# Kernel optimization log

Measured on AMD Instinct MI355X. Metric: run time of the kernel, lower is better.

Reference implementation:

```python
import jax, jax.numpy as jnp
import numpy as np

NF = 64      # feature channels of h
K = 3        # dynamic filter spatial size (padding=1 in source implies k=3)
FACTOR = 4   # pixel-unshuffle factor


def shuffle_down(x, f):
    # torch pixel_unshuffle: (B,C,H*f,W*f) -> (B,C*f*f,H,W)
    B, C, H, W = x.shape
    x = x.reshape(B, C, H // f, f, W // f, f)
    x = x.transpose(0, 1, 3, 5, 2, 4)
    return x.reshape(B, C * f * f, H // f, W // f)


def _patches3x3(x):
    # x: (B,C,H,W) -> (B,C,9,H,W): zero-padded 3x3 neighborhoods, row-major taps,
    # identical to the identity-filter grouped conv (im2col) in the source.
    H, W = x.shape[-2], x.shape[-1]
    xp = jnp.pad(x, ((0, 0), (0, 0), (1, 1), (1, 1)))
    shifts = [xp[:, :, dy:dy + H, dx:dx + W] for dy in range(K) for dx in range(K)]
    return jnp.stack(shifts, axis=2)


def setup_inputs() -> dict:
    key = jax.random.key(0)
    k1, k2, k3, k4 = jax.random.split(key, 4)
    B, H, W = 2, 256, 256
    h = jax.random.normal(k1, (B, NF, H, W), dtype=jnp.float32)
    i_t = jax.random.normal(k2, (B, 3, H * FACTOR, W * FACTOR), dtype=jnp.float32)
    conv_w = jax.random.normal(k3, (K * K, 3 * FACTOR ** 2, K, K), dtype=jnp.float32) * 0.05
    conv_b = jax.random.normal(k4, (K * K,), dtype=jnp.float32) * 0.05
    return {"h": h, "i_t": i_t, "conv_w": conv_w, "conv_b": conv_b}


def reference(h, i_t, conv_w, conv_b):
    # predict per-pixel 3x3 filters from the shuffled-down guidance frame
    x = shuffle_down(i_t, FACTOR)  # (B, 48, H, W)
    f = jax.lax.conv_general_dilated(
        x, conv_w, window_strides=(1, 1), padding=((1, 1), (1, 1)),
        dimension_numbers=("NCHW", "OIHW", "NCHW"))
    filters = jax.nn.relu(f + conv_b[None, :, None, None])  # (B, 9, H, W)

    # dynamic per-pixel conv: same 3x3 filter applied to every channel of h
    patches = _patches3x3(h)  # (B, nf, 9, H, W)
    out = jnp.einsum("bcfhw,bfhw->bchw", patches, filters)  # (B, nf, H, W)
    return out
```

## Files before the change

### kernel.cpp

```cpp
#include <hip/hip_runtime.h>

#define HSZ 256
#define WSZ 256
#define NFC 64
#define PLANE (HSZ * WSZ)

typedef __attribute__((ext_vector_type(8))) short short8;
typedef __attribute__((ext_vector_type(4))) float f32x4;

__device__ inline unsigned short f2bf(float f) {
    unsigned u = __builtin_bit_cast(unsigned, f);
    return (unsigned short)((u + 0x7fffu + ((u >> 16) & 1u)) >> 16);
}

__global__ __launch_bounds__(256, 3) void fused_dynfilter_v2(
    const float* __restrict__ hbuf,
    const float* __restrict__ i_t,
    const float* __restrict__ wbuf,
    const float* __restrict__ bias,
    float* __restrict__ out)
{
    __shared__ __align__(16) unsigned char smem[45504];
    unsigned short* const xs = (unsigned short*)smem;
    unsigned short* const lw = (unsigned short*)(smem + 36288);
    float* const lf = (float*)(smem + 36288);
    float* const hs = (float*)smem;

    const int tid  = threadIdx.x;
    const int X0   = blockIdx.x * 16;
    const int Y0   = blockIdx.y * 16;
    const int b    = blockIdx.z;
    const int lane = tid & 63;
    const int l15  = lane & 15;
    const int kg   = lane >> 4;
    const int wv   = tid >> 6;

    const float bv = (l15 < 9) ? bias[l15] : 0.f;
    const float* itb = i_t + (size_t)b * 3 * (PLANE * 16);

    {
#pragma unroll
        for (int g = 0; g < 2; ++g) {
            float4 lreg[8]; int sdst[8];
#pragma unroll
            for (int k = 0; k < 8; ++k) {
                const int v = tid + 256 * (g * 8 + k);
                const int sp = v / 12, t = v - sp * 12;
                const int c3 = t >> 2, fy = t & 3;
                const int ly = sp / 18, lx = sp - ly * 18;
                const int Y = Y0 - 1 + ly, X = X0 - 1 + lx;
                float4 val = make_float4(0.f, 0.f, 0.f, 0.f);
                if (v < 3888 && (unsigned)Y < HSZ && (unsigned)X < WSZ)
                    val = *(const float4*)(itb + ((size_t)c3 * 1024 + (4 * Y + fy)) * 1024 + 4 * X);
                lreg[k] = val;
                sdst[k] = (v < 3888) ? (sp * 56 + t * 4) : -1;
            }
#pragma unroll
            for (int k = 0; k < 8; ++k)
                if (sdst[k] >= 0) {
                    ushort4 u{f2bf(lreg[k].x), f2bf(lreg[k].y), f2bf(lreg[k].z), f2bf(lreg[k].w)};
                    *(ushort4*)(xs + sdst[k]) = u;
                }
        }
    }

    {
        float wreg[16]; int wdst[16];
#pragma unroll
        for (int k = 0; k < 16; ++k) {
            const int v = tid + 256 * k;
            float w = 0.f; int d = -1;
            if (v < 3888) {
                const int oc = v / 432, kc = v - 432 * oc;
                const int kk = kc / 48, ic = kc - 48 * kk;
                w = wbuf[oc * 432 + ic * 9 + kk];
                d = kc * 9 + oc;
            }
            wreg[k] = w; wdst[k] = d;
        }
#pragma unroll
        for (int k = 0; k < 16; ++k)
            if (wdst[k] >= 0) lw[wdst[k]] = f2bf(wreg[k]);
    }

    __syncthreads();

    short8 wf[14];
    {
        const int base = kg * 72 + l15;
#pragma unroll
        for (int kb = 0; kb < 14; ++kb) {
            unsigned short v8[8];
#pragma unroll
            for (int j = 0; j < 8; ++j)
                v8[j] = lw[base + (kb * 32 + j) * 9];
            if (kb == 13 && kg >= 2) {
#pragma unroll
                for (int j = 0; j < 8; ++j) v8[j] = 0;
            }
            short8 w;
#pragma unroll
            for (int j = 0; j < 8; ++j) w[j] = (short)v8[j];
            wf[kb] = w;
        }
    }

    f32x4 acc[4];
#pragma unroll
    for (int t = 0; t < 4; ++t) acc[t] = (f32x4){0.f, 0.f, 0.f, 0.f};

#pragma unroll
    for (int kb = 0; kb < 14; ++kb) {
        const int k0 = kb * 32 + kg * 8;
        int off = 0;
        if (k0 < 432) {
            const int kk = k0 / 48, ic0 = k0 - 48 * kk;
            const int ky = kk / 3, kx = kk - 3 * ky;
            off = ((4 * wv + ky) * 18 + l15 + kx) * 56 + ic0;
        }
        const unsigned short* ap = xs + off;
#pragma unroll
        for (int t = 0; t < 4; ++t) {
            short8 a = *(const short8*)(ap + t * 1008);
            acc[t] = __builtin_amdgcn_mfma_f32_16x16x32_bf16(a, wf[kb], acc[t], 0, 0, 0);
        }
    }

    __syncthreads();

    if (l15 < 9) {
#pragma unroll
        for (int t = 0; t < 4; ++t) {
            const int py = 4 * wv + t;
#pragma unroll
            for (int r = 0; r < 4; ++r)
                lf[l15 * 256 + py * 16 + (kg * 4 + r)] = fmaxf(acc[t][r] + bv, 0.f);
        }
    }

    const int pq  = tid & 3;
    const int pyA = (tid >> 2) & 15;
    const int clo = tid >> 6;

    float4 h0reg[4]; int h0dst[4];
    {
        const float* hp = hbuf + (size_t)b * NFC * PLANE;
#pragma unroll
        for (int k = 0; k < 4; ++k) {
            const int v = tid + 256 * k;
            float4 val = make_float4(0.f, 0.f, 0.f, 0.f);
            int d = -1;
            if (v < 864) {
                const int c = v / 108, r = v - 108 * c;
                const int row = r / 6, xq = r - 6 * row;
                const int Y = Y0 - 1 + row, X4 = X0 - 4 + xq * 4;
                if ((unsigned)Y < HSZ && (unsigned)X4 < WSZ)
                    val = *(const float4*)(hp + (size_t)c * PLANE + (size_t)Y * WSZ + X4);
                d = c * 432 + row * 24 + xq * 4;
            }
            h0reg[k] = val; h0dst[k] = d;
        }
    }

    __syncthreads();

    float4 flt[9];
#pragma unroll
    for (int oc = 0; oc < 9; ++oc)
        flt[oc] = *(const float4*)(lf + oc * 256 + pyA * 16 + pq * 4);

#pragma unroll
    for (int k = 0; k < 4; ++k)
        if (h0dst[k] >= 0) *(float4*)(hs + h0dst[k]) = h0reg[k];

    __syncthreads();

#pragma unroll
    for (int cg = 0; cg < 8; ++cg) {
        const int buf = cg & 1;

        float4 nreg[4]; int ndst[4];
        if (cg < 7) {
            const float* hp = hbuf + ((size_t)b * NFC + (cg + 1) * 8) * PLANE;
#pragma unroll
            for (int k = 0; k < 4; ++k) {
                const int v = tid + 256 * k;
                float4 val = make_float4(0.f, 0.f, 0.f, 0.f);
                int d = -1;
                if (v < 864) {
                    const int c = v / 108, r = v - 108 * c;
                    const int row = r / 6, xq = r - 6 * row;
                    const int Y = Y0 - 1 + row, X4 = X0 - 4 + xq * 4;
                    if ((unsigned)Y < HSZ && (unsigned)X4 < WSZ)
                        val = *(const float4*)(hp + (size_t)c * PLANE + (size_t)Y * WSZ + X4);
                    d = c * 432 + row * 24 + xq * 4;
                }
                nreg[k] = val; ndst[k] = d;
            }
        }

        float a[2][4];
#pragma unroll
        for (int cc = 0; cc < 2; ++cc)
#pragma unroll
            for (int j = 0; j < 4; ++j) a[cc][j] = 0.f;

#pragma unroll
        for (int cc = 0; cc < 2; ++cc) {
            const float* pl = hs + buf * 3456 + (clo * 2 + cc) * 432;
#pragma unroll
            for (int ky = 0; ky < 3; ++ky) {
                const float* rp = pl + (pyA + ky) * 24 + pq * 4;
                const float4 w0 = *(const float4*)rp;
                const float4 w1 = *(const float4*)(rp + 4);
                const float w8 = rp[8];
                const float vs[9] = {w0.x, w0.y, w0.z, w0.w, w1.x, w1.y, w1.z, w1.w, w8};
#pragma unroll
                for (int kx = 0; kx < 3; ++kx)
#pragma unroll
                    for (int j = 0; j < 4; ++j)
                        a[cc][j] = fmaf(vs[3 + kx + j], flt[ky * 3 + kx][j], a[cc][j]);
            }
        }

#pragma unroll
        for (int cc = 0; cc < 2; ++cc) {
            const int ch = cg * 8 + clo * 2 + cc;
            *(float4*)(out + ((size_t)b * NFC + ch) * PLANE
                           + (size_t)(Y0 + pyA) * WSZ + X0 + pq * 4)
                = make_float4(a[cc][0], a[cc][1], a[cc][2], a[cc][3]);
        }

        if (cg < 7) {
            float* hb = hs + (buf ^ 1) * 3456;
#pragma unroll
            for (int k = 0; k < 4; ++k)
                if (ndst[k] >= 0) *(float4*)(hb + ndst[k]) = nreg[k];
            __syncthreads();
        }
    }
}

extern "C" void kernel_launch(void* const* d_in, const int* in_sizes, int n_in,
                              void* d_out, int out_size, void* d_ws, size_t ws_size,
                              hipStream_t stream) {
    const float* h      = (const float*)d_in[0];
    const float* i_t    = (const float*)d_in[1];
    const float* conv_w = (const float*)d_in[2];
    const float* conv_b = (const float*)d_in[3];
    float* out = (float*)d_out;

    const int B = in_sizes[0] / (NFC * PLANE);
    dim3 grid(WSZ / 16, HSZ / 16, B);
    fused_dynfilter_v2<<<grid, 256, 0, stream>>>(h, i_t, conv_w, conv_b, out);
}
```

Baseline: 125.0 us.

## Halve tile height, remap blocks XCD-aware, and vectorize weight staging

Shrinks each block's tile from 16x16 to 16x8 pixels, which cuts shared memory from about 45KB to 28KB and raises launch bounds to 4 blocks per SM. Block ids are remapped so that consecutive tiles land on the same XCD, aiming at better L2 reuse of halos. Weights are now loaded as float4 and stored transposed, so each MFMA B-fragment is one short8 LDS read instead of eight scattered reads. The cost is more halo overhead per output pixel and twice as many blocks, so each block repeats the weight staging.

```diff
diff --git a/kernel.cpp b/kernel.cpp
--- a/kernel.cpp
+++ b/kernel.cpp
@@ -13,23 +13,29 @@
     return (unsigned short)((u + 0x7fffu + ((u >> 16) & 1u)) >> 16);
 }
 
-__global__ __launch_bounds__(256, 3) void fused_dynfilter_v2(
+__global__ __launch_bounds__(256, 4) void fused_dynfilter_v3(
     const float* __restrict__ hbuf,
     const float* __restrict__ i_t,
     const float* __restrict__ wbuf,
     const float* __restrict__ bias,
     float* __restrict__ out)
 {
-    __shared__ __align__(16) unsigned char smem[45504];
-    unsigned short* const xs = (unsigned short*)smem;
-    unsigned short* const lw = (unsigned short*)(smem + 36288);
-    float* const lf = (float*)(smem + 36288);
+    __shared__ __align__(16) unsigned char smem[28096];
+    unsigned short* const xs  = (unsigned short*)smem;
+    unsigned short* const lwT = (unsigned short*)(smem + 20160);
+    float* const lf = (float*)(smem + 20160);
     float* const hs = (float*)smem;
 
-    const int tid  = threadIdx.x;
-    const int X0   = blockIdx.x * 16;
-    const int Y0   = blockIdx.y * 16;
-    const int b    = blockIdx.z;
+    const int tid = threadIdx.x;
+
+    const int lin = blockIdx.x + 16 * (blockIdx.y + 32 * blockIdx.z);
+    const int q   = ((int)gridDim.z * 512) >> 3;
+    const int nid = (lin & 7) * q + (lin >> 3);
+    const int b   = nid >> 9;
+    const int rem = nid & 511;
+    const int X0  = (rem & 15) * 16;
+    const int Y0  = (rem >> 4) * 8;
+
     const int lane = tid & 63;
     const int l15  = lane & 15;
     const int kg   = lane >> 4;
@@ -39,76 +45,69 @@
     const float* itb = i_t + (size_t)b * 3 * (PLANE * 16);
 
     {
-#pragma unroll
-        for (int g = 0; g < 2; ++g) {
-            float4 lreg[8]; int sdst[8];
-#pragma unroll
-            for (int k = 0; k < 8; ++k) {
-                const int v = tid + 256 * (g * 8 + k);
-                const int sp = v / 12, t = v - sp * 12;
-                const int c3 = t >> 2, fy = t & 3;
-                const int ly = sp / 18, lx = sp - ly * 18;
-                const int Y = Y0 - 1 + ly, X = X0 - 1 + lx;
-                float4 val = make_float4(0.f, 0.f, 0.f, 0.f);
-                if (v < 3888 && (unsigned)Y < HSZ && (unsigned)X < WSZ)
-                    val = *(const float4*)(itb + ((size_t)c3 * 1024 + (4 * Y + fy)) * 1024 + 4 * X);
-                lreg[k] = val;
-                sdst[k] = (v < 3888) ? (sp * 56 + t * 4) : -1;
-            }
-#pragma unroll
-            for (int k = 0; k < 8; ++k)
-                if (sdst[k] >= 0) {
-                    ushort4 u{f2bf(lreg[k].x), f2bf(lreg[k].y), f2bf(lreg[k].z), f2bf(lreg[k].w)};
-                    *(ushort4*)(xs + sdst[k]) = u;
+        float4 lreg[9]; int sdst[9];
+#pragma unroll
+        for (int k = 0; k < 9; ++k) {
+            const int v = tid + 256 * k;
+            const int sp = v / 12, t = v - sp * 12;
+            const int c3 = t >> 2, fy = t & 3;
+            const int ly = sp / 18, lx = sp - ly * 18;
+            const int Y = Y0 - 1 + ly, X = X0 - 1 + lx;
+            float4 val = make_float4(0.f, 0.f, 0.f, 0.f);
+            if (v < 2160 && (unsigned)Y < HSZ && (unsigned)X < WSZ)
+                val = *(const float4*)(itb + ((size_t)c3 * 1024 + (4 * Y + fy)) * 1024 + 4 * X);
+            lreg[k] = val;
+            sdst[k] = (v < 2160) ? (sp * 56 + t * 4) : -1;
+        }
+#pragma unroll
+        for (int k = 0; k < 9; ++k)
+            if (sdst[k] >= 0) {
+                ushort4 u{f2bf(lreg[k].x), f2bf(lreg[k].y), f2bf(lreg[k].z), f2bf(lreg[k].w)};
+                *(ushort4*)(xs + sdst[k]) = u;
+            }
+    }
+
+    {
+        float4 wr[4];
+#pragma unroll
+        for (int k = 0; k < 4; ++k) {
+            const int v = tid + 256 * k;
+            wr[k] = (v < 972) ? *(const float4*)(wbuf + (size_t)v * 4)
+                              : make_float4(0.f, 0.f, 0.f, 0.f);
+        }
+#pragma unroll
+        for (int k = 0; k < 4; ++k) {
+            const int v = tid + 256 * k;
+            if (v < 972) {
+                const float e[4] = {wr[k].x, wr[k].y, wr[k].z, wr[k].w};
+#pragma unroll
+                for (int j = 0; j < 4; ++j) {
+                    const int n  = v * 4 + j;
+                    const int oc = n / 432;
+                    const int r  = n - 432 * oc;
+                    const int ic = r / 9;
+                    const int kk = r - 9 * ic;
+                    lwT[oc * 440 + kk * 48 + ic] = f2bf(e[j]);
                 }
-        }
-    }
-
-    {
-        float wreg[16]; int wdst[16];
-#pragma unroll
-        for (int k = 0; k < 16; ++k) {
-            const int v = tid + 256 * k;
-            float w = 0.f; int d = -1;
-            if (v < 3888) {
-                const int oc = v / 432, kc = v - 432 * oc;
-                const int kk = kc / 48, ic = kc - 48 * kk;
-                w = wbuf[oc * 432 + ic * 9 + kk];
-                d = kc * 9 + oc;
-            }
-            wreg[k] = w; wdst[k] = d;
-        }
-#pragma unroll
-        for (int k = 0; k < 16; ++k)
-            if (wdst[k] >= 0) lw[wdst[k]] = f2bf(wreg[k]);
+            }
+        }
     }
 
     __syncthreads();
 
     short8 wf[14];
     {
-        const int base = kg * 72 + l15;
+        const unsigned short* lwb = lwT + l15 * 440 + kg * 8;
 #pragma unroll
         for (int kb = 0; kb < 14; ++kb) {
-            unsigned short v8[8];
-#pragma unroll
-            for (int j = 0; j < 8; ++j)
-                v8[j] = lw[base + (kb * 32 + j) * 9];
-            if (kb == 13 && kg >= 2) {
-#pragma unroll
-                for (int j = 0; j < 8; ++j) v8[j] = 0;
-            }
-            short8 w;
-#pragma unroll
-            for (int j = 0; j < 8; ++j) w[j] = (short)v8[j];
+            short8 w = {0, 0, 0, 0, 0, 0, 0, 0};
+            if (l15 < 9 && !(kb == 13 && kg >= 2))
+                w = *(const short8*)(lwb + kb * 32);
             wf[kb] = w;
         }
     }
 
-    f32x4 acc[4];
-#pragma unroll
-    for (int t = 0; t < 4; ++t) acc[t] = (f32x4){0.f, 0.f, 0.f, 0.f};
-
+    f32x4 acc0 = {0.f, 0.f, 0.f, 0.f}, acc1 = acc0;
 #pragma unroll
     for (int kb = 0; kb < 14; ++kb) {
         const int k0 = kb * 32 + kg * 8;
@@ -116,47 +115,46 @@
         if (k0 < 432) {
             const int kk = k0 / 48, ic0 = k0 - 48 * kk;
             const int ky = kk / 3, kx = kk - 3 * ky;
-            off = ((4 * wv + ky) * 18 + l15 + kx) * 56 + ic0;
-        }
-        const unsigned short* ap = xs + off;
-#pragma unroll
-        for (int t = 0; t < 4; ++t) {
-            short8 a = *(const short8*)(ap + t * 1008);
-            acc[t] = __builtin_amdgcn_mfma_f32_16x16x32_bf16(a, wf[kb], acc[t], 0, 0, 0);
-        }
+            off = ((2 * wv + ky) * 18 + l15 + kx) * 56 + ic0;
+        }
+        short8 a0 = *(const short8*)(xs + off);
+        short8 a1 = *(const short8*)(xs + off + 1008);
+        acc0 = __builtin_amdgcn_mfma_f32_16x16x32_bf16(a0, wf[kb], acc0, 0, 0, 0);
+        acc1 = __builtin_amdgcn_mfma_f32_16x16x32_bf16(a1, wf[kb], acc1, 0, 0, 0);
     }
 
     __syncthreads();
 
     if (l15 < 9) {
 #pragma unroll
-        for (int t = 0; t < 4; ++t) {
-            const int py = 4 * wv + t;
+        for (int t = 0; t < 2; ++t) {
+            const int py = 2 * wv + t;
+            const f32x4 A = t ? acc1 : acc0;
 #pragma unroll
             for (int r = 0; r < 4; ++r)
-                lf[l15 * 256 + py * 16 + (kg * 4 + r)] = fmaxf(acc[t][r] + bv, 0.f);
+                lf[l15 * 128 + py * 16 + (kg * 4 + r)] = fmaxf(A[r] + bv, 0.f);
         }
     }
 
     const int pq  = tid & 3;
-    const int pyA = (tid >> 2) & 15;
-    const int clo = tid >> 6;
-
-    float4 h0reg[4]; int h0dst[4];
+    const int pyA = (tid >> 2) & 7;
+    const int clo = tid >> 5;
+
+    float4 h0reg[2]; int h0dst[2];
     {
         const float* hp = hbuf + (size_t)b * NFC * PLANE;
 #pragma unroll
-        for (int k = 0; k < 4; ++k) {
+        for (int k = 0; k < 2; ++k) {
             const int v = tid + 256 * k;
             float4 val = make_float4(0.f, 0.f, 0.f, 0.f);
             int d = -1;
-            if (v < 864) {
-                const int c = v / 108, r = v - 108 * c;
+            if (v < 480) {
+                const int c = v / 60, r = v - 60 * c;
                 const int row = r / 6, xq = r - 6 * row;
                 const int Y = Y0 - 1 + row, X4 = X0 - 4 + xq * 4;
                 if ((unsigned)Y < HSZ && (unsigned)X4 < WSZ)
                     val = *(const float4*)(hp + (size_t)c * PLANE + (size_t)Y * WSZ + X4);
-                d = c * 432 + row * 24 + xq * 4;
+                d = c * 240 + row * 24 + xq * 4;
             }
             h0reg[k] = val; h0dst[k] = d;
         }
@@ -167,10 +165,10 @@
     float4 flt[9];
 #pragma unroll
     for (int oc = 0; oc < 9; ++oc)
-        flt[oc] = *(const float4*)(lf + oc * 256 + pyA * 16 + pq * 4);
-
-#pragma unroll
-    for (int k = 0; k < 4; ++k)
+        flt[oc] = *(const float4*)(lf + oc * 128 + pyA * 16 + pq * 4);
+
+#pragma unroll
+    for (int k = 0; k < 2; ++k)
         if (h0dst[k] >= 0) *(float4*)(hs + h0dst[k]) = h0reg[k];
 
     __syncthreads();
@@ -179,62 +177,54 @@
     for (int cg = 0; cg < 8; ++cg) {
         const int buf = cg & 1;
 
-        float4 nreg[4]; int ndst[4];
+        float4 nreg[2]; int ndst[2];
         if (cg < 7) {
             const float* hp = hbuf + ((size_t)b * NFC + (cg + 1) * 8) * PLANE;
 #pragma unroll
-            for (int k = 0; k < 4; ++k) {
+            for (int k = 0; k < 2; ++k) {
                 const int v = tid + 256 * k;
                 float4 val = make_float4(0.f, 0.f, 0.f, 0.f);
                 int d = -1;
-                if (v < 864) {
-                    const int c = v / 108, r = v - 108 * c;
+                if (v < 480) {
+                    const int c = v / 60, r = v - 60 * c;
                     const int row = r / 6, xq = r - 6 * row;
                     const int Y = Y0 - 1 + row, X4 = X0 - 4 + xq * 4;
                     if ((unsigned)Y < HSZ && (unsigned)X4 < WSZ)
                         val = *(const float4*)(hp + (size_t)c * PLANE + (size_t)Y * WSZ + X4);
-                    d = c * 432 + row * 24 + xq * 4;
+                    d = c * 240 + row * 24 + xq * 4;
                 }
                 nreg[k] = val; ndst[k] = d;
             }
         }
 
-        float a[2][4];
-#pragma unroll
-        for (int cc = 0; cc < 2; ++cc)
-#pragma unroll
-            for (int j = 0; j < 4; ++j) a[cc][j] = 0.f;
-
-#pragma unroll
-        for (int cc = 0; cc < 2; ++cc) {
-            const float* pl = hs + buf * 3456 + (clo * 2 + cc) * 432;
-#pragma unroll
-            for (int ky = 0; ky < 3; ++ky) {
-                const float* rp = pl + (pyA + ky) * 24 + pq * 4;
-                const float4 w0 = *(const float4*)rp;
-                const float4 w1 = *(const float4*)(rp + 4);
-                const float w8 = rp[8];
-                const float vs[9] = {w0.x, w0.y, w0.z, w0.w, w1.x, w1.y, w1.z, w1.w, w8};
-#pragma unroll
-                for (int kx = 0; kx < 3; ++kx)
-#pragma unroll
-                    for (int j = 0; j < 4; ++j)
-                        a[cc][j] = fmaf(vs[3 + kx + j], flt[ky * 3 + kx][j], a[cc][j]);
-            }
-        }
-
-#pragma unroll
-        for (int cc = 0; cc < 2; ++cc) {
-            const int ch = cg * 8 + clo * 2 + cc;
-            *(float4*)(out + ((size_t)b * NFC + ch) * PLANE
-                           + (size_t)(Y0 + pyA) * WSZ + X0 + pq * 4)
-                = make_float4(a[cc][0], a[cc][1], a[cc][2], a[cc][3]);
-        }
+        float a[4];
+#pragma unroll
+        for (int j = 0; j < 4; ++j) a[j] = 0.f;
+
+        const float* pl = hs + buf * 1920 + clo * 240;
+#pragma unroll
+        for (int ky = 0; ky < 3; ++ky) {
+            const float* rp = pl + (pyA + ky) * 24 + pq * 4;
+            const float4 w0 = *(const float4*)rp;
+            const float4 w1 = *(const float4*)(rp + 4);
+            const float  w8 = rp[8];
+            const float vs[9] = {w0.x, w0.y, w0.z, w0.w, w1.x, w1.y, w1.z, w1.w, w8};
+#pragma unroll
+            for (int kx = 0; kx < 3; ++kx)
+#pragma unroll
+                for (int j = 0; j < 4; ++j)
+                    a[j] = fmaf(vs[3 + kx + j], flt[ky * 3 + kx][j], a[j]);
+        }
+
+        const int ch = cg * 8 + clo;
+        *(float4*)(out + ((size_t)b * NFC + ch) * PLANE
+                       + (size_t)(Y0 + pyA) * WSZ + X0 + pq * 4)
+            = make_float4(a[0], a[1], a[2], a[3]);
 
         if (cg < 7) {
-            float* hb = hs + (buf ^ 1) * 3456;
-#pragma unroll
-            for (int k = 0; k < 4; ++k)
+            float* hb = hs + (buf ^ 1) * 1920;
+#pragma unroll
+            for (int k = 0; k < 2; ++k)
                 if (ndst[k] >= 0) *(float4*)(hb + ndst[k]) = nreg[k];
             __syncthreads();
         }
@@ -251,6 +241,6 @@
     float* out = (float*)d_out;
 
     const int B = in_sizes[0] / (NFC * PLANE);
-    dim3 grid(WSZ / 16, HSZ / 16, B);
-    fused_dynfilter_v2<<<grid, 256, 0, stream>>>(h, i_t, conv_w, conv_b, out);
+    dim3 grid(WSZ / 16, HSZ / 8, B);
+    fused_dynfilter_v3<<<grid, 256, 0, stream>>>(h, i_t, conv_w, conv_b, out);
 }
```

After: 116.9 us. 1.07x faster.
